# Optimization experiments

Measured on AMD Instinct MI355X. Metric: run time of the kernel, lower is better.

## Reference

```python
import jax, jax.numpy as jnp
import numpy as np

GROUPS = 8
EPS = 1e-3  # keras GroupNormalization default epsilon


def group_norm(x, gamma, beta):
    # x: [B,H,W,C], groups over channel axis
    B, H, W, C = x.shape
    g = GROUPS
    xr = x.reshape(B, H, W, g, C // g)
    mean = jnp.mean(xr, axis=(1, 2, 4), keepdims=True)
    var = jnp.var(xr, axis=(1, 2, 4), keepdims=True)
    xn = (xr - mean) * jax.lax.rsqrt(var + EPS)
    xn = xn.reshape(B, H, W, C)
    return xn * gamma + beta


def setup_inputs() -> dict:
    key = jax.random.key(0)
    ks = jax.random.split(key, 6)
    B, H, W, C = 8, 64, 64, 64
    std = 0.02
    return {
        "x": jax.random.normal(ks[0], (B, H, W, C), dtype=jnp.float32),
        "gamma": jnp.ones((C,), dtype=jnp.float32),
        "beta": jnp.zeros((C,), dtype=jnp.float32),
        "wq": jax.random.normal(ks[1], (C, C), dtype=jnp.float32) * std,
        "bq": jnp.zeros((C,), dtype=jnp.float32),
        "wk": jax.random.normal(ks[2], (C, C), dtype=jnp.float32) * std,
        "bk": jnp.zeros((C,), dtype=jnp.float32),
        "wv": jax.random.normal(ks[3], (C, C), dtype=jnp.float32) * std,
        "bv": jnp.zeros((C,), dtype=jnp.float32),
        "wp": jax.random.normal(ks[4], (C, C), dtype=jnp.float32) * std,
        "bp": jnp.zeros((C,), dtype=jnp.float32),
    }


def reference(x, gamma, beta, wq, bq, wk, bk, wv, bv, wp, bp):
    B, H, W, C = x.shape
    scale = jnp.asarray(C, x.dtype) ** -0.5
    h = group_norm(x, gamma, beta)  # note: residual uses normalized input (as in source)
    q = h @ wq + bq
    k = h @ wk + bk
    v = h @ wv + bv
    # full O((HW)^2) score tensor, exactly as the original
    attn = jnp.einsum('bhwc,bHWc->bhwHW', q, k) * scale
    attn = jax.nn.softmax(attn.reshape(B, H, W, H * W), axis=-1)
    attn = attn.reshape(B, H, W, H, W)
    proj = jnp.einsum('bhwHW,bHWc->bhwc', attn, v)
    proj = proj @ wp + bp
    return h + proj
```

## Files before the change

### kernel.cpp

```cpp
#include <hip/hip_runtime.h>

#define NTOK 4096
#define CH 64
#define LOG2E 1.4426950408889634f
#define QK_SCALE 0.42466090014400953f

typedef __bf16 bf8 __attribute__((ext_vector_type(8)));
typedef __bf16 bf4 __attribute__((ext_vector_type(4)));
typedef _Float16 h8 __attribute__((ext_vector_type(8)));
typedef _Float16 h4 __attribute__((ext_vector_type(4)));
typedef float f4 __attribute__((ext_vector_type(4)));
typedef long lx2 __attribute__((ext_vector_type(2)));

__device__ __forceinline__ f4 mfma16(bf8 a, bf8 b, f4 c) {
    return __builtin_amdgcn_mfma_f32_16x16x32_bf16(a, b, c, 0, 0, 0);
}
__device__ __forceinline__ f4 mfma8(long a, long b, f4 c) {
    return __builtin_amdgcn_mfma_f32_16x16x32_fp8_fp8(a, b, c, 0, 0, 0);
}
__device__ __forceinline__ unsigned char to_fp8(float v) {
    return (unsigned char)(__builtin_amdgcn_cvt_pk_fp8_f32(v, v, 0, false) & 0xff);
}
__device__ __forceinline__ float fexp2(float x) {
    return __int_as_float((int)fmaf(x, 8388608.f, 1064985795.f));
}

__global__ __launch_bounds__(256) void pre_kernel(const float* __restrict__ wq,
                                                  const float* __restrict__ wk,
                                                  const float* __restrict__ wv,
                                                  const float* __restrict__ wp,
                                                  const float* __restrict__ x,
                                                  __bf16* __restrict__ wqt,
                                                  __bf16* __restrict__ wkt,
                                                  __bf16* __restrict__ wvt,
                                                  __bf16* __restrict__ wpt,
                                                  float* __restrict__ gpart) {
    int t = threadIdx.x;
    if (blockIdx.x < 4) {
        int m = blockIdx.x;
        const float* src = (m == 0) ? wq : (m == 1) ? wk : (m == 2) ? wv : wp;
        __bf16* dst      = (m == 0) ? wqt : (m == 1) ? wkt : (m == 2) ? wvt : wpt;
        __shared__ float s[64][65];
        for (int i = 0; i < 16; ++i) {
            int e = i * 256 + t;
            s[e >> 6][e & 63] = src[e];
        }
        __syncthreads();
        int o = t >> 2, seg = t & 3;
        for (int j = 0; j < 16; ++j) {
            int in = seg * 16 + j;
            dst[o * 64 + in] = (__bf16)s[in][o];
        }
        return;
    }
    int bid = blockIdx.x - 4;
    int b = bid >> 6, slab = bid & 63;
    const float4* xb = (const float4*)(x + (size_t)(b * NTOK + slab * 64) * CH);
    float s = 0.f, ss = 0.f;
    for (int i = 0; i < 4; ++i) {
        int row = (t >> 4) + i * 16;
        float4 v = xb[row * 16 + (t & 15)];
        s  += v.x + v.y + v.z + v.w;
        ss += v.x * v.x + v.y * v.y + v.z * v.z + v.w * v.w;
    }
    __shared__ float ls[256], lss[256];
    ls[t] = s; lss[t] = ss;
    __syncthreads();
    if (t < 8) {
        float a = 0.f, aa = 0.f;
        for (int p = 0; p < 16; ++p) {
            a  += ls[p * 16 + 2 * t]  + ls[p * 16 + 2 * t + 1];
            aa += lss[p * 16 + 2 * t] + lss[p * 16 + 2 * t + 1];
        }
        gpart[((b * 64 + slab) * 8 + t) * 2 + 0] = a;
        gpart[((b * 64 + slab) * 8 + t) * 2 + 1] = aa;
    }
}

__global__ __launch_bounds__(256) void qkv_gn(const float* __restrict__ x,
                                              const float* __restrict__ gpart,
                                              const float* __restrict__ gamma,
                                              const float* __restrict__ beta,
                                              const __bf16* __restrict__ wqt,
                                              const __bf16* __restrict__ wkt,
                                              const __bf16* __restrict__ wvt,
                                              const float* __restrict__ bq,
                                              const float* __restrict__ bk,
                                              const float* __restrict__ bv,
                                              unsigned char* __restrict__ qp,
                                              unsigned char* __restrict__ kp,
                                              unsigned char* __restrict__ vp) {
    __shared__ __bf16 W[3][64][72];
    __shared__ _Float16 Vst[64][68];
    __shared__ unsigned char Qst[64][72];
    __shared__ unsigned char Kst[64][72];
    __shared__ float red[128];
    __shared__ float sstat[16];
    __shared__ float sg[64], sb2[64];
    int t = threadIdx.x;
    size_t rowbase = (size_t)blockIdx.x * 64;
    int b = (int)(rowbase >> 12), tokbase = (int)(rowbase & 4095);
    int lane = t & 63, wave = t >> 6, quad = lane >> 4, l15 = lane & 15;
    int row = wave * 16 + l15;

    const float* xr = x + (rowbase + row) * 64;
    float4 xl0 = *(const float4*)(xr + quad * 8);
    float4 xl1 = *(const float4*)(xr + quad * 8 + 4);
    float4 xh0 = *(const float4*)(xr + 32 + quad * 8);
    float4 xh1 = *(const float4*)(xr + 32 + quad * 8 + 4);

    for (int m = 0; m < 3; ++m) {
        const __bf16* src = (m == 0) ? wqt : (m == 1) ? wkt : wvt;
        for (int i = 0; i < 2; ++i) {
            int e = i * 256 + t, rr = e >> 3, ch = e & 7;
            *(bf8*)&W[m][rr][ch * 8] = *(const bf8*)(src + rr * 64 + ch * 8);
        }
    }
    if (t < 64) { sg[t] = gamma[t]; sb2[t] = beta[t]; }
    if (t < 64) {
        int gi = t & 7, c = t >> 3;
        const float2* gp = (const float2*)gpart + (size_t)b * 512 + gi;
        float a = 0.f, aa = 0.f;
        for (int p = c * 8; p < c * 8 + 8; ++p) {
            float2 v = gp[(size_t)p * 8];
            a += v.x; aa += v.y;
        }
        red[t * 2] = a; red[t * 2 + 1] = aa;
    }
    __syncthreads();
    if (t < 8) {
        float a = 0.f, aa = 0.f;
        for (int c = 0; c < 8; ++c) {
            a  += red[(c * 8 + t) * 2];
            aa += red[(c * 8 + t) * 2 + 1];
        }
        float mean = a * (1.f / 32768.f);
        float var = aa * (1.f / 32768.f) - mean * mean;
        sstat[t * 2 + 0] = mean;
        sstat[t * 2 + 1] = rsqrtf(var + 1e-3f);
    }
    __syncthreads();

    bf8 a0, a1;
    {
        float mlo = sstat[quad * 2], rlo = sstat[quad * 2 + 1];
        float mhi = sstat[(4 + quad) * 2], rhi = sstat[(4 + quad) * 2 + 1];
        float xl[8] = {xl0.x, xl0.y, xl0.z, xl0.w, xl1.x, xl1.y, xl1.z, xl1.w};
        float xh[8] = {xh0.x, xh0.y, xh0.z, xh0.w, xh1.x, xh1.y, xh1.z, xh1.w};
#pragma unroll
        for (int j = 0; j < 8; ++j) {
            int c = quad * 8 + j;
            a0[j] = (__bf16)((xl[j] - mlo) * sg[c] * rlo + sb2[c]);
            a1[j] = (__bf16)((xh[j] - mhi) * sg[32 + c] * rhi + sb2[32 + c]);
        }
    }

    for (int m = 0; m < 3; ++m) {
        const float* bias = (m == 0) ? bq : (m == 1) ? bk : bv;
        float sc = (m == 2) ? 1.0f : QK_SCALE;
        for (int tt = 0; tt < 4; ++tt) {
            int col = l15 + 16 * tt;
            bf8 b0 = *(const bf8*)&W[m][col][quad * 8];
            bf8 b1 = *(const bf8*)&W[m][col][32 + quad * 8];
            f4 acc = {0.f, 0.f, 0.f, 0.f};
            acc = mfma16(a0, b0, acc);
            acc = mfma16(a1, b1, acc);
            float bb = bias[col];
            if (m == 2) {
                for (int r = 0; r < 4; ++r)
                    Vst[col][wave * 16 + quad * 4 + r] = (_Float16)(acc[r] + bb);
            } else if (m == 1) {
                for (int r = 0; r < 4; ++r)
                    Kst[wave * 16 + quad * 4 + r][col] = to_fp8((acc[r] + bb) * sc);
            } else {
                for (int r = 0; r < 4; ++r)
                    Qst[wave * 16 + quad * 4 + r][col] = to_fp8((acc[r] + bb) * sc);
            }
        }
    }
    __syncthreads();
    {
        const unsigned char* krow = &Kst[wave * 16 + l15][0];
        lx2 kk; kk[0] = *(const long*)(krow + quad * 8);
        kk[1] = *(const long*)(krow + 32 + quad * 8);
        *(lx2*)(kp + (((size_t)b * 256 + (tokbase >> 4) + wave) * 64 + lane) * 16) = kk;
        const unsigned char* qrow = &Qst[wave * 16 + l15][0];
        lx2 qq; qq[0] = *(const long*)(qrow + quad * 8);
        qq[1] = *(const long*)(qrow + 32 + quad * 8);
        *(lx2*)(qp + (((size_t)b * 256 + (tokbase >> 4) + wave) * 64 + lane) * 16) = qq;
    }
    {
        int d = wave * 16 + l15;
        for (int kb = 0; kb < 2; ++kb) {
            h4 lo = *(const h4*)&Vst[d][kb * 32 + quad * 4];
            h4 hi = *(const h4*)&Vst[d][kb * 32 + 16 + quad * 4];
            int d0 = __builtin_amdgcn_cvt_pk_fp8_f32((float)lo[0], (float)lo[1], 0, false);
            d0     = __builtin_amdgcn_cvt_pk_fp8_f32((float)lo[2], (float)lo[3], d0, true);
            int d1 = __builtin_amdgcn_cvt_pk_fp8_f32((float)hi[0], (float)hi[1], 0, false);
            d1     = __builtin_amdgcn_cvt_pk_fp8_f32((float)hi[2], (float)hi[3], d1, true);
            long v8 = (long)(unsigned int)d0 | ((long)d1 << 32);
            int kt = (tokbase >> 5) + kb;
            *(long*)(vp + ((((size_t)b * 128 + kt) * 2 + (wave >> 1)) * 64 + lane) * 16
                        + (wave & 1) * 8) = v8;
        }
    }
}

__device__ __forceinline__ void load_kv(const unsigned char* kpw, const unsigned char* vpw,
                                        long kf[4], long vf[4]) {
    lx2 a = *(const lx2*)(kpw);
    lx2 b = *(const lx2*)(kpw + 1024);
    lx2 c = *(const lx2*)(vpw);
    lx2 d = *(const lx2*)(vpw + 1024);
    kf[0] = a[0]; kf[1] = a[1]; kf[2] = b[0]; kf[3] = b[1];
    vf[0] = c[0]; vf[1] = c[1]; vf[2] = d[0]; vf[3] = d[1];
}

__device__ __forceinline__ void compute32(const long kf[4], const long vf[4],
                                          const long aqlo[8], const long aqhi[8],
                                          long ones, f4 acc[8][4], f4 acc_li[8]) {
#pragma unroll
    for (int s = 0; s < 8; ++s) {
        f4 St0 = {0.f, 0.f, 0.f, 0.f};
        f4 St1 = {0.f, 0.f, 0.f, 0.f};
        St0 = mfma8(kf[0], aqlo[s], St0);
        St0 = mfma8(kf[1], aqhi[s], St0);
        St1 = mfma8(kf[2], aqlo[s], St1);
        St1 = mfma8(kf[3], aqhi[s], St1);
        float p00 = fexp2(St0[0]);
        float p01 = fexp2(St0[1]);
        float p02 = fexp2(St0[2]);
        float p03 = fexp2(St0[3]);
        float p10 = fexp2(St1[0]);
        float p11 = fexp2(St1[1]);
        float p12 = fexp2(St1[2]);
        float p13 = fexp2(St1[3]);
        int d0 = __builtin_amdgcn_cvt_pk_fp8_f32(p00, p01, 0, false);
        d0     = __builtin_amdgcn_cvt_pk_fp8_f32(p02, p03, d0, true);
        int d1 = __builtin_amdgcn_cvt_pk_fp8_f32(p10, p11, 0, false);
        d1     = __builtin_amdgcn_cvt_pk_fp8_f32(p12, p13, d1, true);
        long pf = (long)(unsigned int)d0 | ((long)d1 << 32);
        acc_li[s] = mfma8(ones, pf, acc_li[s]);
        acc[s][0] = mfma8(vf[0], pf, acc[s][0]);
        acc[s][1] = mfma8(vf[1], pf, acc[s][1]);
        acc[s][2] = mfma8(vf[2], pf, acc[s][2]);
        acc[s][3] = mfma8(vf[3], pf, acc[s][3]);
    }
}

__global__ __launch_bounds__(512, 1) void attn_final(const unsigned char* __restrict__ qp,
                                                     const unsigned char* __restrict__ kp,
                                                     const unsigned char* __restrict__ vp,
                                                     const __bf16* __restrict__ wpt,
                                                     const float* __restrict__ bp,
                                                     const float* __restrict__ x,
                                                     const float* __restrict__ gpart,
                                                     const float* __restrict__ gamma,
                                                     const float* __restrict__ beta,
                                                     float* __restrict__ out) {
    __shared__ _Float16 Om[4][128][72];
    __shared__ float sS[4][128];
    __shared__ __bf16 Wl[64][72];
    __shared__ __bf16 Ol[128][72];
    __shared__ float red[128];
    __shared__ float sstat[16], sg[64], sb[64];

    int bid = blockIdx.x;
    int qt = bid >> 3, b = bid & 7;
    int t = threadIdx.x, lane = t & 63, w = t >> 6, quad = lane >> 4, l15 = lane & 15;

    {
        int row = t >> 3, ch = t & 7;
        *(bf8*)&Wl[row][ch * 8] = *(const bf8*)(wpt + row * 64 + ch * 8);
    }
    if (t >= 64 && t < 128) { int u = t - 64; sg[u] = gamma[u]; sb[u] = beta[u]; }
    if (t < 64) {
        int gi = t & 7, c = t >> 3;
        const float2* gp = (const float2*)gpart + (size_t)b * 512 + gi;
        float a = 0.f, aa = 0.f;
        for (int p = c * 8; p < c * 8 + 8; ++p) {
            float2 v = gp[(size_t)p * 8];
            a += v.x; aa += v.y;
        }
        red[t * 2] = a; red[t * 2 + 1] = aa;
    }

    const unsigned char* qpb = qp + (((size_t)b * 256 + qt * 8) * 64 + lane) * 16;
    long aqlo[8], aqhi[8];
#pragma unroll
    for (int s = 0; s < 8; ++s) {
        lx2 qq = *(const lx2*)(qpb + (size_t)s * 1024);
        aqlo[s] = qq[0]; aqhi[s] = qq[1];
    }
    const unsigned char* kpw = kp + ((size_t)b * 256 + w * 32) * 1024 + lane * 16;
    const unsigned char* vpw = vp + ((size_t)b * 128 + w * 16) * 2048 + lane * 16;

    const long ones = 0x3838383838383838L;

    f4 acc[8][4] = {};
    f4 acc_li[8] = {};

    long kfA[4], kfB[4], vfA[4], vfB[4];
    load_kv(kpw, vpw, kfA, vfA);
    for (int it = 0; it < 16; it += 2) {
        load_kv(kpw + (size_t)(it + 1) * 2048, vpw + (size_t)(it + 1) * 2048, kfB, vfB);
        __builtin_amdgcn_s_setprio(1);
        compute32(kfA, vfA, aqlo, aqhi, ones, acc, acc_li);
        __builtin_amdgcn_s_setprio(0);
        if (it + 2 < 16)
            load_kv(kpw + (size_t)(it + 2) * 2048, vpw + (size_t)(it + 2) * 2048, kfA, vfA);
        __builtin_amdgcn_s_setprio(1);
        compute32(kfB, vfB, aqlo, aqhi, ones, acc, acc_li);
        __builtin_amdgcn_s_setprio(0);
    }

    float li[8];
#pragma unroll
    for (int s = 0; s < 8; ++s) li[s] = acc_li[s][0];

    if (w >= 4) {
        for (int s = 0; s < 8; ++s) {
            for (int td = 0; td < 4; ++td) {
                h4 o4;
                for (int r = 0; r < 4; ++r) o4[r] = (_Float16)acc[s][td][r];
                *(h4*)&Om[w - 4][s * 16 + l15][td * 16 + quad * 4] = o4;
            }
            if (quad == 0) sS[w - 4][s * 16 + l15] = li[s];
        }
    }
    __syncthreads();
    if (t < 8) {
        float a = 0.f, aa = 0.f;
        for (int c = 0; c < 8; ++c) {
            a  += red[(c * 8 + t) * 2];
            aa += red[(c * 8 + t) * 2 + 1];
        }
        float mean = a * (1.f / 32768.f);
        float var = aa * (1.f / 32768.f) - mean * mean;
        sstat[t * 2 + 0] = mean;
        sstat[t * 2 + 1] = rsqrtf(var + 1e-3f);
    }
    if (w < 4) {
        for (int s = 0; s < 8; ++s) {
            for (int td = 0; td < 4; ++td) {
                h4 o4 = *(const h4*)&Om[w][s * 16 + l15][td * 16 + quad * 4];
                for (int r = 0; r < 4; ++r) acc[s][td][r] += (float)o4[r];
            }
            li[s] += sS[w][s * 16 + l15];
        }
    }
    __syncthreads();
    if (w >= 2 && w < 4) {
        for (int s = 0; s < 8; ++s) {
            for (int td = 0; td < 4; ++td) {
                h4 o4;
                for (int r = 0; r < 4; ++r) o4[r] = (_Float16)acc[s][td][r];
                *(h4*)&Om[w - 2][s * 16 + l15][td * 16 + quad * 4] = o4;
            }
            if (quad == 0) sS[w - 2][s * 16 + l15] = li[s];
        }
    }
    __syncthreads();
    if (w < 2) {
        for (int s = 0; s < 8; ++s) {
            for (int td = 0; td < 4; ++td) {
                h4 o4 = *(const h4*)&Om[w][s * 16 + l15][td * 16 + quad * 4];
                for (int r = 0; r < 4; ++r) acc[s][td][r] += (float)o4[r];
            }
            li[s] += sS[w][s * 16 + l15];
        }
    }
    __syncthreads();
    if (w < 2) {
        for (int s = 0; s < 8; ++s) {
            for (int td = 0; td < 4; ++td) {
                h4 o4;
                for (int r = 0; r < 4; ++r) o4[r] = (_Float16)acc[s][td][r];
                *(h4*)&Om[w][s * 16 + l15][td * 16 + quad * 4] = o4;
            }
            if (quad == 0) sS[w][s * 16 + l15] = li[s];
        }
    }
    __syncthreads();
    {
        int qq = t >> 2, ds = (t & 3) * 16;
        float inv = 1.f / (sS[0][qq] + sS[1][qq]);
        h8 a0 = *(const h8*)&Om[0][qq][ds];
        h8 b0 = *(const h8*)&Om[0][qq][ds + 8];
        h8 a1 = *(const h8*)&Om[1][qq][ds];
        h8 b1 = *(const h8*)&Om[1][qq][ds + 8];
        bf8 olo, ohi;
        for (int j = 0; j < 8; ++j) {
            olo[j] = (__bf16)(((float)a0[j] + (float)a1[j]) * inv);
            ohi[j] = (__bf16)(((float)b0[j] + (float)b1[j]) * inv);
        }
        *(bf8*)&Ol[qq][ds] = olo;
        *(bf8*)&Ol[qq][ds + 8] = ohi;
    }
    __syncthreads();
    {
        size_t rowbase = ((size_t)b * NTOK + qt * 128) + w * 16;
        bf8 a0 = *(const bf8*)&Ol[w * 16 + l15][quad * 8];
        bf8 a1 = *(const bf8*)&Ol[w * 16 + l15][32 + quad * 8];
        for (int tt = 0; tt < 4; ++tt) {
            int col = l15 + 16 * tt;
            bf8 b0 = *(const bf8*)&Wl[col][quad * 8];
            bf8 b1 = *(const bf8*)&Wl[col][32 + quad * 8];
            f4 pacc = {0.f, 0.f, 0.f, 0.f};
            pacc = mfma16(a0, b0, pacc);
            pacc = mfma16(a1, b1, pacc);
            int grp = col >> 3;
            float mean = sstat[grp * 2], gs = sg[col] * sstat[grp * 2 + 1], bs = sb[col];
            float bias = bp[col];
            for (int r = 0; r < 4; ++r) {
                size_t gi = (rowbase + quad * 4 + r) * 64 + col;
                float h = (x[gi] - mean) * gs + bs;
                out[gi] = pacc[r] + bias + h;
            }
        }
    }
}

extern "C" void kernel_launch(void* const* d_in, const int* in_sizes, int n_in,
                              void* d_out, int out_size, void* d_ws, size_t ws_size,
                              hipStream_t stream) {
    const float* x     = (const float*)d_in[0];
    const float* gamma = (const float*)d_in[1];
    const float* beta  = (const float*)d_in[2];
    const float* wq    = (const float*)d_in[3];
    const float* bq    = (const float*)d_in[4];
    const float* wk    = (const float*)d_in[5];
    const float* bk    = (const float*)d_in[6];
    const float* wv    = (const float*)d_in[7];
    const float* bv    = (const float*)d_in[8];
    const float* wp    = (const float*)d_in[9];
    const float* bp    = (const float*)d_in[10];
    float* out = (float*)d_out;

    char* ws = (char*)d_ws;
    const size_t MB = 1024 * 1024;
    unsigned char* qpb = (unsigned char*)(ws);
    unsigned char* kpb = (unsigned char*)(ws + 2 * MB);
    unsigned char* vpb = (unsigned char*)(ws + 4 * MB);
    __bf16*   wqt  = (__bf16*)(ws + 12 * MB);
    __bf16*   wkt  = (__bf16*)(ws + 12 * MB + 8192);
    __bf16*   wvt  = (__bf16*)(ws + 12 * MB + 16384);
    __bf16*   wpt  = (__bf16*)(ws + 12 * MB + 24576);
    float*    gpart = (float*)(ws + 12 * MB + 32768);

    pre_kernel<<<516, 256, 0, stream>>>(wq, wk, wv, wp, x, wqt, wkt, wvt, wpt, gpart);
    qkv_gn<<<512, 256, 0, stream>>>(x, gpart, gamma, beta, wqt, wkt, wvt, bq, bk, bv,
                                    qpb, kpb, vpb);
    attn_final<<<256, 512, 0, stream>>>(qpb, kpb, vpb, wpt, bp, x, gpart, gamma, beta, out);
}
```

Before: 120.0 us.

## Switch attention core to 32x32x64 scaled FP8 MFMA with relaid Q/K/V packing

Replaces the 16x16x32 fp8 MFMA attention loop with the gfx950 scaled 32x32x64 f8f6f4 MFMA, using unit scales. Q, K and V are repacked in the producer kernel into 32-token tiles that match the larger instruction's operand layout. The row-sum is now accumulated in VALU adds plus a cross-half shuffle instead of an extra MFMA against a ones vector. This cuts the MFMA instruction count and operand traffic per tile. In exchange it uses larger accumulator register tiles, drops the double-buffered K/V prefetch, and changes the reduction layout.

```diff
diff --git a/kernel.cpp b/kernel.cpp
--- a/kernel.cpp
+++ b/kernel.cpp
@@ -10,19 +10,31 @@
 typedef _Float16 h8 __attribute__((ext_vector_type(8)));
 typedef _Float16 h4 __attribute__((ext_vector_type(4)));
 typedef float f4 __attribute__((ext_vector_type(4)));
+typedef float fx16 __attribute__((ext_vector_type(16)));
+typedef int ix4 __attribute__((ext_vector_type(4)));
+typedef int ix8 __attribute__((ext_vector_type(8)));
 typedef long lx2 __attribute__((ext_vector_type(2)));
 
 __device__ __forceinline__ f4 mfma16(bf8 a, bf8 b, f4 c) {
     return __builtin_amdgcn_mfma_f32_16x16x32_bf16(a, b, c, 0, 0, 0);
 }
-__device__ __forceinline__ f4 mfma8(long a, long b, f4 c) {
-    return __builtin_amdgcn_mfma_f32_16x16x32_fp8_fp8(a, b, c, 0, 0, 0);
+__device__ __forceinline__ fx16 mfma_mx(ix8 a, ix8 b, fx16 c) {
+    return __builtin_amdgcn_mfma_scale_f32_32x32x64_f8f6f4(
+        a, b, c, 0, 0, 0, 0x7F7F7F7F, 0, 0x7F7F7F7F);
 }
 __device__ __forceinline__ unsigned char to_fp8(float v) {
     return (unsigned char)(__builtin_amdgcn_cvt_pk_fp8_f32(v, v, 0, false) & 0xff);
 }
 __device__ __forceinline__ float fexp2(float x) {
     return __int_as_float((int)fmaf(x, 8388608.f, 1064985795.f));
+}
+__device__ __forceinline__ ix8 load32(const unsigned char* p) {
+    ix4 lo = *(const ix4*)p;
+    ix4 hi = *(const ix4*)(p + 16);
+    ix8 r;
+    r[0] = lo[0]; r[1] = lo[1]; r[2] = lo[2]; r[3] = lo[3];
+    r[4] = hi[0]; r[5] = hi[1]; r[6] = hi[2]; r[7] = hi[3];
+    return r;
 }
 
 __global__ __launch_bounds__(256) void pre_kernel(const float* __restrict__ wq,
@@ -92,8 +104,8 @@
                                               unsigned char* __restrict__ vp) {
     __shared__ __bf16 W[3][64][72];
     __shared__ _Float16 Vst[64][68];
-    __shared__ unsigned char Qst[64][72];
-    __shared__ unsigned char Kst[64][72];
+    __shared__ unsigned char Qst[64][80];
+    __shared__ unsigned char Kst[64][80];
     __shared__ float red[128];
     __shared__ float sstat[16];
     __shared__ float sg[64], sb2[64];
@@ -180,71 +192,31 @@
     }
     __syncthreads();
     {
-        const unsigned char* krow = &Kst[wave * 16 + l15][0];
-        lx2 kk; kk[0] = *(const long*)(krow + quad * 8);
-        kk[1] = *(const long*)(krow + 32 + quad * 8);
-        *(lx2*)(kp + (((size_t)b * 256 + (tokbase >> 4) + wave) * 64 + lane) * 16) = kk;
-        const unsigned char* qrow = &Qst[wave * 16 + l15][0];
-        lx2 qq; qq[0] = *(const long*)(qrow + quad * 8);
-        qq[1] = *(const long*)(qrow + 32 + quad * 8);
-        *(lx2*)(qp + (((size_t)b * 256 + (tokbase >> 4) + wave) * 64 + lane) * 16) = qq;
-    }
-    {
-        int d = wave * 16 + l15;
-        for (int kb = 0; kb < 2; ++kb) {
-            h4 lo = *(const h4*)&Vst[d][kb * 32 + quad * 4];
-            h4 hi = *(const h4*)&Vst[d][kb * 32 + 16 + quad * 4];
-            int d0 = __builtin_amdgcn_cvt_pk_fp8_f32((float)lo[0], (float)lo[1], 0, false);
-            d0     = __builtin_amdgcn_cvt_pk_fp8_f32((float)lo[2], (float)lo[3], d0, true);
-            int d1 = __builtin_amdgcn_cvt_pk_fp8_f32((float)hi[0], (float)hi[1], 0, false);
-            d1     = __builtin_amdgcn_cvt_pk_fp8_f32((float)hi[2], (float)hi[3], d1, true);
-            long v8 = (long)(unsigned int)d0 | ((long)d1 << 32);
-            int kt = (tokbase >> 5) + kb;
-            *(long*)(vp + ((((size_t)b * 128 + kt) * 2 + (wave >> 1)) * 64 + lane) * 16
-                        + (wave & 1) * 8) = v8;
-        }
-    }
-}
-
-__device__ __forceinline__ void load_kv(const unsigned char* kpw, const unsigned char* vpw,
-                                        long kf[4], long vf[4]) {
-    lx2 a = *(const lx2*)(kpw);
-    lx2 b = *(const lx2*)(kpw + 1024);
-    lx2 c = *(const lx2*)(vpw);
-    lx2 d = *(const lx2*)(vpw + 1024);
-    kf[0] = a[0]; kf[1] = a[1]; kf[2] = b[0]; kf[3] = b[1];
-    vf[0] = c[0]; vf[1] = c[1]; vf[2] = d[0]; vf[3] = d[1];
-}
-
-__device__ __forceinline__ void compute32(const long kf[4], const long vf[4],
-                                          const long aqlo[8], const long aqhi[8],
-                                          long ones, f4 acc[8][4], f4 acc_li[8]) {
-#pragma unroll
-    for (int s = 0; s < 8; ++s) {
-        f4 St0 = {0.f, 0.f, 0.f, 0.f};
-        f4 St1 = {0.f, 0.f, 0.f, 0.f};
-        St0 = mfma8(kf[0], aqlo[s], St0);
-        St0 = mfma8(kf[1], aqhi[s], St0);
-        St1 = mfma8(kf[2], aqlo[s], St1);
-        St1 = mfma8(kf[3], aqhi[s], St1);
-        float p00 = fexp2(St0[0]);
-        float p01 = fexp2(St0[1]);
-        float p02 = fexp2(St0[2]);
-        float p03 = fexp2(St0[3]);
-        float p10 = fexp2(St1[0]);
-        float p11 = fexp2(St1[1]);
-        float p12 = fexp2(St1[2]);
-        float p13 = fexp2(St1[3]);
-        int d0 = __builtin_amdgcn_cvt_pk_fp8_f32(p00, p01, 0, false);
-        d0     = __builtin_amdgcn_cvt_pk_fp8_f32(p02, p03, d0, true);
-        int d1 = __builtin_amdgcn_cvt_pk_fp8_f32(p10, p11, 0, false);
-        d1     = __builtin_amdgcn_cvt_pk_fp8_f32(p12, p13, d1, true);
-        long pf = (long)(unsigned int)d0 | ((long)d1 << 32);
-        acc_li[s] = mfma8(ones, pf, acc_li[s]);
-        acc[s][0] = mfma8(vf[0], pf, acc[s][0]);
-        acc[s][1] = mfma8(vf[1], pf, acc[s][1]);
-        acc[s][2] = mfma8(vf[2], pf, acc[s][2]);
-        acc[s][3] = mfma8(vf[3], pf, acc[s][3]);
+        int slot = t >> 1, hb = t & 1;
+        int tile = slot >> 6, ln = slot & 63;
+        int rr = tile * 32 + (ln & 31), h = ln >> 5;
+        size_t dst = (((size_t)b * 128 + (tokbase >> 5) + tile) * 64 + ln) * 32 + hb * 16;
+        *(lx2*)(kp + dst) = *(const lx2*)&Kst[rr][h * 32 + hb * 16];
+        *(lx2*)(qp + dst) = *(const lx2*)&Qst[rr][h * 32 + hb * 16];
+    }
+    {
+        int dt = t >> 7, ln = (t >> 1) & 63, kb = t & 1;
+        int d = dt * 32 + (ln & 31), h = ln >> 5;
+        unsigned int dw[4];
+#pragma unroll
+        for (int g = 0; g < 4; ++g) {
+            int k0 = kb * 32 + 4 * h + 8 * g;
+            int dd = __builtin_amdgcn_cvt_pk_fp8_f32((float)Vst[d][k0 + 0],
+                                                     (float)Vst[d][k0 + 1], 0, false);
+            dd     = __builtin_amdgcn_cvt_pk_fp8_f32((float)Vst[d][k0 + 2],
+                                                     (float)Vst[d][k0 + 3], dd, true);
+            dw[g] = (unsigned int)dd;
+        }
+        lx2 vv;
+        vv[0] = (long)dw[0] | ((long)dw[1] << 32);
+        vv[1] = (long)dw[2] | ((long)dw[3] << 32);
+        *(lx2*)(vp + ((((size_t)b * 64 + (tokbase >> 6)) * 2 + dt) * 64 + ln) * 32
+                   + kb * 16) = vv;
     }
 }
 
@@ -268,6 +240,7 @@
     int bid = blockIdx.x;
     int qt = bid >> 3, b = bid & 7;
     int t = threadIdx.x, lane = t & 63, w = t >> 6, quad = lane >> 4, l15 = lane & 15;
+    int l31 = lane & 31, hh = lane >> 5;
 
     {
         int row = t >> 3, ch = t & 7;
@@ -285,47 +258,75 @@
         red[t * 2] = a; red[t * 2 + 1] = aa;
     }
 
-    const unsigned char* qpb = qp + (((size_t)b * 256 + qt * 8) * 64 + lane) * 16;
-    long aqlo[8], aqhi[8];
-#pragma unroll
-    for (int s = 0; s < 8; ++s) {
-        lx2 qq = *(const lx2*)(qpb + (size_t)s * 1024);
-        aqlo[s] = qq[0]; aqhi[s] = qq[1];
-    }
-    const unsigned char* kpw = kp + ((size_t)b * 256 + w * 32) * 1024 + lane * 16;
-    const unsigned char* vpw = vp + ((size_t)b * 128 + w * 16) * 2048 + lane * 16;
-
-    const long ones = 0x3838383838383838L;
-
-    f4 acc[8][4] = {};
-    f4 acc_li[8] = {};
-
-    long kfA[4], kfB[4], vfA[4], vfB[4];
-    load_kv(kpw, vpw, kfA, vfA);
-    for (int it = 0; it < 16; it += 2) {
-        load_kv(kpw + (size_t)(it + 1) * 2048, vpw + (size_t)(it + 1) * 2048, kfB, vfB);
+    const unsigned char* qpb = qp + (((size_t)b * 128 + qt * 4) * 64 + lane) * 32;
+    ix8 Qf[4];
+#pragma unroll
+    for (int s = 0; s < 4; ++s) Qf[s] = load32(qpb + (size_t)s * 2048);
+    const unsigned char* kpw = kp + (((size_t)b * 128 + w * 16) * 64 + lane) * 32;
+    const unsigned char* vpw = vp + (((size_t)b * 64 + w * 8) * 2 * 64 + lane) * 32;
+
+    fx16 acc[2][4] = {};
+    float li[4] = {0.f, 0.f, 0.f, 0.f};
+    const fx16 fz = {};
+
+    for (int it = 0; it < 8; ++it) {
+        const unsigned char* kpt = kpw + (size_t)it * 4096;
+        const unsigned char* vpt = vpw + (size_t)it * 4096;
+        ix8 K0 = load32(kpt);
+        ix8 K1 = load32(kpt + 2048);
+        ix8 V0 = load32(vpt);
+        ix8 V1 = load32(vpt + 2048);
         __builtin_amdgcn_s_setprio(1);
-        compute32(kfA, vfA, aqlo, aqhi, ones, acc, acc_li);
+#pragma unroll
+        for (int s = 0; s < 4; ++s) {
+            fx16 St0 = mfma_mx(K0, Qf[s], fz);
+            fx16 St1 = mfma_mx(K1, Qf[s], fz);
+            ix8 pf;
+#pragma unroll
+            for (int g = 0; g < 4; ++g) {
+                float p0 = fexp2(St0[4 * g + 0]);
+                float p1 = fexp2(St0[4 * g + 1]);
+                float p2 = fexp2(St0[4 * g + 2]);
+                float p3 = fexp2(St0[4 * g + 3]);
+                li[s] += (p0 + p1) + (p2 + p3);
+                int dd = __builtin_amdgcn_cvt_pk_fp8_f32(p0, p1, 0, false);
+                dd     = __builtin_amdgcn_cvt_pk_fp8_f32(p2, p3, dd, true);
+                pf[g] = dd;
+            }
+#pragma unroll
+            for (int g = 0; g < 4; ++g) {
+                float p0 = fexp2(St1[4 * g + 0]);
+                float p1 = fexp2(St1[4 * g + 1]);
+                float p2 = fexp2(St1[4 * g + 2]);
+                float p3 = fexp2(St1[4 * g + 3]);
+                li[s] += (p0 + p1) + (p2 + p3);
+                int dd = __builtin_amdgcn_cvt_pk_fp8_f32(p0, p1, 0, false);
+                dd     = __builtin_amdgcn_cvt_pk_fp8_f32(p2, p3, dd, true);
+                pf[4 + g] = dd;
+            }
+            acc[0][s] = mfma_mx(V0, pf, acc[0][s]);
+            acc[1][s] = mfma_mx(V1, pf, acc[1][s]);
+        }
         __builtin_amdgcn_s_setprio(0);
-        if (it + 2 < 16)
-            load_kv(kpw + (size_t)(it + 2) * 2048, vpw + (size_t)(it + 2) * 2048, kfA, vfA);
-        __builtin_amdgcn_s_setprio(1);
-        compute32(kfB, vfB, aqlo, aqhi, ones, acc, acc_li);
-        __builtin_amdgcn_s_setprio(0);
-    }
-
-    float li[8];
-#pragma unroll
-    for (int s = 0; s < 8; ++s) li[s] = acc_li[s][0];
+    }
+
+#pragma unroll
+    for (int s = 0; s < 4; ++s) li[s] += __shfl_xor(li[s], 32);
 
     if (w >= 4) {
-        for (int s = 0; s < 8; ++s) {
-            for (int td = 0; td < 4; ++td) {
-                h4 o4;
-                for (int r = 0; r < 4; ++r) o4[r] = (_Float16)acc[s][td][r];
-                *(h4*)&Om[w - 4][s * 16 + l15][td * 16 + quad * 4] = o4;
-            }
-            if (quad == 0) sS[w - 4][s * 16 + l15] = li[s];
+#pragma unroll
+        for (int s = 0; s < 4; ++s) {
+            int q = s * 32 + l31;
+#pragma unroll
+            for (int dt = 0; dt < 2; ++dt)
+#pragma unroll
+                for (int g = 0; g < 4; ++g) {
+                    h4 o4;
+#pragma unroll
+                    for (int r = 0; r < 4; ++r) o4[r] = (_Float16)acc[dt][s][4 * g + r];
+                    *(h4*)&Om[w - 4][q][dt * 32 + 4 * hh + 8 * g] = o4;
+                }
+            if (lane < 32) sS[w - 4][q] = li[s];
         }
     }
     __syncthreads();
@@ -341,44 +342,68 @@
         sstat[t * 2 + 1] = rsqrtf(var + 1e-3f);
     }
     if (w < 4) {
-        for (int s = 0; s < 8; ++s) {
-            for (int td = 0; td < 4; ++td) {
-                h4 o4 = *(const h4*)&Om[w][s * 16 + l15][td * 16 + quad * 4];
-                for (int r = 0; r < 4; ++r) acc[s][td][r] += (float)o4[r];
-            }
-            li[s] += sS[w][s * 16 + l15];
+#pragma unroll
+        for (int s = 0; s < 4; ++s) {
+            int q = s * 32 + l31;
+#pragma unroll
+            for (int dt = 0; dt < 2; ++dt)
+#pragma unroll
+                for (int g = 0; g < 4; ++g) {
+                    h4 o4 = *(const h4*)&Om[w][q][dt * 32 + 4 * hh + 8 * g];
+#pragma unroll
+                    for (int r = 0; r < 4; ++r) acc[dt][s][4 * g + r] += (float)o4[r];
+                }
+            li[s] += sS[w][q];
         }
     }
     __syncthreads();
     if (w >= 2 && w < 4) {
-        for (int s = 0; s < 8; ++s) {
-            for (int td = 0; td < 4; ++td) {
-                h4 o4;
-                for (int r = 0; r < 4; ++r) o4[r] = (_Float16)acc[s][td][r];
-                *(h4*)&Om[w - 2][s * 16 + l15][td * 16 + quad * 4] = o4;
-            }
-            if (quad == 0) sS[w - 2][s * 16 + l15] = li[s];
+#pragma unroll
+        for (int s = 0; s < 4; ++s) {
+            int q = s * 32 + l31;
+#pragma unroll
+            for (int dt = 0; dt < 2; ++dt)
+#pragma unroll
+                for (int g = 0; g < 4; ++g) {
+                    h4 o4;
+#pragma unroll
+                    for (int r = 0; r < 4; ++r) o4[r] = (_Float16)acc[dt][s][4 * g + r];
+                    *(h4*)&Om[w - 2][q][dt * 32 + 4 * hh + 8 * g] = o4;
+                }
+            if (lane < 32) sS[w - 2][q] = li[s];
         }
     }
     __syncthreads();
     if (w < 2) {
-        for (int s = 0; s < 8; ++s) {
-            for (int td = 0; td < 4; ++td) {
-                h4 o4 = *(const h4*)&Om[w][s * 16 + l15][td * 16 + quad * 4];
-                for (int r = 0; r < 4; ++r) acc[s][td][r] += (float)o4[r];
-            }
-            li[s] += sS[w][s * 16 + l15];
+#pragma unroll
+        for (int s = 0; s < 4; ++s) {
+            int q = s * 32 + l31;
+#pragma unroll
+            for (int dt = 0; dt < 2; ++dt)
+#pragma unroll
+                for (int g = 0; g < 4; ++g) {
+                    h4 o4 = *(const h4*)&Om[w][q][dt * 32 + 4 * hh + 8 * g];
+#pragma unroll
+                    for (int r = 0; r < 4; ++r) acc[dt][s][4 * g + r] += (float)o4[r];
+                }
+            li[s] += sS[w][q];
         }
     }
     __syncthreads();
     if (w < 2) {
-        for (int s = 0; s < 8; ++s) {
-            for (int td = 0; td < 4; ++td) {
-                h4 o4;
-                for (int r = 0; r < 4; ++r) o4[r] = (_Float16)acc[s][td][r];
-                *(h4*)&Om[w][s * 16 + l15][td * 16 + quad * 4] = o4;
-            }
-            if (quad == 0) sS[w][s * 16 + l15] = li[s];
+#pragma unroll
+        for (int s = 0; s < 4; ++s) {
+            int q = s * 32 + l31;
+#pragma unroll
+            for (int dt = 0; dt < 2; ++dt)
+#pragma unroll
+                for (int g = 0; g < 4; ++g) {
+                    h4 o4;
+#pragma unroll
+                    for (int r = 0; r < 4; ++r) o4[r] = (_Float16)acc[dt][s][4 * g + r];
+                    *(h4*)&Om[w][q][dt * 32 + 4 * hh + 8 * g] = o4;
+                }
+            if (lane < 32) sS[w][q] = li[s];
         }
     }
     __syncthreads();
```

After: 119.8 us. No clear change (-0.2%).
